# Kernel tuning notes

Measured on AMD Instinct MI355X. Metric: run time of the kernel, lower is better.

Reference implementation:

```python
import jax, jax.numpy as jnp
import numpy as np

K = 10                # knn neighbors
HEADS = 4             # attention heads
NAMES = ["self", "cross", "self", "cross", "self", "cross"]
SINKHORN_ITERS = 10


def _knn_graph_feature(x, k):
    # x: (b, c, n) -> (b, 2c, n, k), DGCNN-style graph feature
    xx = jnp.sum(x * x, axis=1)                              # (b, n)
    inner = jnp.einsum('bcn,bcm->bnm', x, x)
    dist = -xx[:, :, None] + 2.0 * inner - xx[:, None, :]    # negative squared L2
    idx = jax.lax.top_k(dist, k)[1]                          # (b, n, k)
    xt = jnp.transpose(x, (0, 2, 1))                         # (b, n, c)
    nbr = jax.vmap(lambda pts, id_: pts[id_])(xt, idx)       # (b, n, k, c)
    ctr = jnp.broadcast_to(xt[:, :, None, :], nbr.shape)
    feat = jnp.concatenate([nbr - ctr, ctr], axis=-1)        # (b, n, k, 2c)
    return jnp.transpose(feat, (0, 3, 1, 2))


def _encode(pts, w, b):
    # knn_feature: graph feature -> 1x1 conv2d -> mean over neighbors
    f = _knn_graph_feature(pts, K)                           # (b, 2c, n, k)
    y = jnp.einsum('oc,bcnk->bonk', w, f) + b[None, :, None, None]
    return y.mean(axis=-1)                                   # (b, d, n)


def _conv1(x, w, b):
    # 1x1 Conv1d
    return jnp.einsum('od,bdn->bon', w, x) + b[None, :, None]


def _bn(x, g, bt):
    # BatchNorm1d, training-mode batch statistics (biased var), eps=1e-5
    m = x.mean(axis=(0, 2), keepdims=True)
    v = ((x - m) ** 2).mean(axis=(0, 2), keepdims=True)
    return g[None, :, None] * (x - m) / jnp.sqrt(v + 1e-5) + bt[None, :, None]


def _mha(x, src, pw, pb, mw, mb):
    b, d, n = x.shape
    dim = d // HEADS
    q = _conv1(x, pw[0], pb[0]).reshape(b, dim, HEADS, -1)
    k = _conv1(src, pw[1], pb[1]).reshape(b, dim, HEADS, -1)
    v = _conv1(src, pw[2], pb[2]).reshape(b, dim, HEADS, -1)
    scores = jnp.einsum('bdhn,bdhm->bhnm', q, k) / (dim ** 0.5)
    prob = jax.nn.softmax(scores, axis=-1)
    out = jnp.einsum('bhnm,bdhm->bdhn', prob, v).reshape(b, d, -1)
    return _conv1(out, mw, mb)


def _prop(x, src, p):
    # AttentionalPropagation: MHA message + MLP([2d, 2d, d]) with BN+ReLU
    msg = _mha(x, src, p['pw'], p['pb'], p['mw'], p['mb'])
    y = jnp.concatenate([x, msg], axis=1)                    # (b, 2d, n)
    h = jax.nn.relu(_bn(_conv1(y, p['w1'], p['b1']), p['g'], p['bt']))
    return _conv1(h, p['w2'], p['b2'])


def _rodrigues(aa):
    # angle-axis (b,3) -> rotation matrices (b,3,3)
    theta = jnp.maximum(jnp.linalg.norm(aa, axis=-1, keepdims=True), 1e-8)
    r = aa / theta
    c = jnp.cos(theta)[..., None]
    s = jnp.sin(theta)[..., None]
    rx, ry, rz = r[..., 0], r[..., 1], r[..., 2]
    z = jnp.zeros_like(rx)
    Kmat = jnp.stack([jnp.stack([z, -rz, ry], -1),
                      jnp.stack([rz, z, -rx], -1),
                      jnp.stack([-ry, rx, z], -1)], -2)
    rrT = r[..., :, None] * r[..., None, :]
    I = jnp.eye(3, dtype=aa.dtype)
    return c * I + (1.0 - c) * rrT + s * Kmat


def reference(p2d, p3d, pose, enc2d_w, enc2d_b, enc3d_w, enc3d_b,
              proj_w, proj_b, merge_w, merge_b,
              mlp1_w, mlp1_b, bn_g, bn_b, mlp2_w, mlp2_b):
    # unit bearing vectors (assumption stated in weightedReprojectionErrorwithPose)
    f2 = p2d / jnp.linalg.norm(p2d, axis=-1, keepdims=True)
    desc0 = _encode(jnp.transpose(f2, (0, 2, 1)), enc2d_w, enc2d_b)   # (b, d, m)
    desc1 = _encode(jnp.transpose(p3d, (0, 2, 1)), enc3d_w, enc3d_b)  # (b, d, n)

    for i, name in enumerate(NAMES):
        p = dict(pw=proj_w[i], pb=proj_b[i], mw=merge_w[i], mb=merge_b[i],
                 w1=mlp1_w[i], b1=mlp1_b[i], g=bn_g[i], bt=bn_b[i],
                 w2=mlp2_w[i], b2=mlp2_b[i])
        s0, s1 = (desc1, desc0) if name == 'cross' else (desc0, desc1)
        d0 = desc0 + _prop(desc0, s0, p)
        d1 = desc1 + _prop(desc1, s1, p)
        desc0, desc1 = d0, d1

    # pairwiseL2Dist between descriptor sets
    f0 = jnp.transpose(desc0, (0, 2, 1))
    f1 = jnp.transpose(desc1, (0, 2, 1))
    n0 = jnp.sum(f0 * f0, -1)
    n1 = jnp.sum(f1 * f1, -1)
    dist2 = n0[:, :, None] + n1[:, None, :] - 2.0 * jnp.einsum('bmd,bnd->bmn', f0, f1)
    M = jnp.sqrt(jnp.clip(dist2, 1e-30, None))

    # log-space sinkhorn normalization -> joint weight matrix W
    log_alpha = -M
    for _ in range(SINKHORN_ITERS):
        log_alpha = log_alpha - jax.nn.logsumexp(log_alpha, axis=2, keepdims=True)
        log_alpha = log_alpha - jax.nn.logsumexp(log_alpha, axis=1, keepdims=True)
    W = jnp.exp(log_alpha)

    # weighted angular reprojection error at given pose (angle-axis + t)
    R = _rodrigues(pose[:, :3])
    t = pose[:, 3:]
    p3dt = jnp.einsum('bij,bnj->bni', R, p3d) + t[:, None, :]
    p3dt = p3dt / jnp.linalg.norm(p3dt, axis=-1, keepdims=True)
    err = jnp.einsum('bmn,bmn->b', W, 1.0 - jnp.einsum('bmd,bnd->bmn', f2, p3dt))
    return err


def setup_inputs() -> dict:
    key = jax.random.key(0)
    ks = jax.random.split(key, 12)
    B, Mpts, Npts, D, L = 4, 1024, 1024, 128, 6
    f = lambda k_, shp: jax.random.normal(k_, shp, dtype=jnp.float32) * 0.05
    return {
        'p2d': jax.random.normal(ks[0], (B, Mpts, 3), jnp.float32),
        'p3d': jax.random.normal(ks[1], (B, Npts, 3), jnp.float32),
        'pose': jax.random.normal(ks[2], (B, 6), jnp.float32) * 0.2,
        'enc2d_w': f(ks[3], (D, 6)), 'enc2d_b': jnp.zeros((D,), jnp.float32),
        'enc3d_w': f(ks[4], (D, 6)), 'enc3d_b': jnp.zeros((D,), jnp.float32),
        'proj_w': f(ks[5], (L, 3, D, D)), 'proj_b': jnp.zeros((L, 3, D), jnp.float32),
        'merge_w': f(ks[6], (L, D, D)), 'merge_b': jnp.zeros((L, D), jnp.float32),
        'mlp1_w': f(ks[7], (L, 2 * D, 2 * D)), 'mlp1_b': jnp.zeros((L, 2 * D), jnp.float32),
        'bn_g': jnp.ones((L, 2 * D), jnp.float32), 'bn_b': jnp.zeros((L, 2 * D), jnp.float32),
        'mlp2_w': f(ks[8], (L, D, 2 * D)), 'mlp2_b': jnp.zeros((L, D), jnp.float32),
    }
```

## Files before the change

kernel.cpp:

```cpp
#include <hip/hip_runtime.h>
#include <hip/hip_bf16.h>

constexpr int B   = 4;
constexpr int N   = 1024;
constexpr int D   = 128;
constexpr int KNN = 10;
constexpr int NH  = 4;

typedef _Float16 half2v __attribute__((ext_vector_type(2)));
typedef _Float16 f16x4  __attribute__((ext_vector_type(4)));
typedef _Float16 f16x8  __attribute__((ext_vector_type(8)));
typedef float    f32x4  __attribute__((ext_vector_type(4)));

static __device__ __forceinline__ half2v pkrtz(float a, float b) {
  return __builtin_bit_cast(half2v, __builtin_amdgcn_cvt_pkrtz(a, b));
}
static __device__ __forceinline__ float h2f(half2v h) {
  return __builtin_bit_cast(float, h);
}

__global__ __launch_bounds__(256) void k_norm2d(const float* __restrict__ p2d,
                                                float* __restrict__ f2) {
  int i = blockIdx.x * 256 + threadIdx.x;
  const float* p = p2d + (size_t)i * 3;
  float x = p[0], y = p[1], z = p[2];
  float inr = 1.f / sqrtf(x * x + y * y + z * z);
  float* o = f2 + (size_t)i * 3;
  o[0] = x * inr; o[1] = y * inr; o[2] = z * inr;
}

__global__ __launch_bounds__(256) void k_encode(const float* __restrict__ pts,
                                                const float* __restrict__ w,
                                                const float* __restrict__ bias,
                                                float* __restrict__ desc) {
  __shared__ float Px[N], Py[N], Pz[N], Xx[N];
  const int t = threadIdx.x;
  const int l = t & 63, wv = t >> 6;
  const int n = blockIdx.x * 4 + wv;
  const int b = blockIdx.y;
  const float* pb = pts + (size_t)b * N * 3;
  for (int i = t; i < N; i += 256) {
    float x = pb[i * 3 + 0], y = pb[i * 3 + 1], z = pb[i * 3 + 2];
    Px[i] = x; Py[i] = y; Pz[i] = z;
    Xx[i] = x * x + y * y + z * z;
  }
  __syncthreads();
  const float cx = Px[n], cy = Py[n], cz = Pz[n], cxx = Xx[n];
  float dist[16];
#pragma unroll
  for (int i = 0; i < 16; ++i) {
    int j = i * 64 + l;
    float ip = cx * Px[j] + cy * Py[j] + cz * Pz[j];
    dist[i] = 2.f * ip - cxx - Xx[j];
  }
  float sx = 0.f, sy = 0.f, sz = 0.f;
#pragma unroll
  for (int kk = 0; kk < KNN; ++kk) {
    float bv = dist[0]; int bi = l;
#pragma unroll
    for (int i = 1; i < 16; ++i) {
      if (dist[i] > bv) { bv = dist[i]; bi = i * 64 + l; }
    }
#pragma unroll
    for (int sft = 1; sft < 64; sft <<= 1) {
      float v2 = __shfl_xor(bv, sft, 64);
      int   i2 = __shfl_xor(bi, sft, 64);
      if (v2 > bv || (v2 == bv && i2 < bi)) { bv = v2; bi = i2; }
    }
    sx += Px[bi]; sy += Py[bi]; sz += Pz[bi];
    if ((bi & 63) == l) {
      int io = bi >> 6;
#pragma unroll
      for (int i = 0; i < 16; ++i)
        if (i == io) dist[i] = -3.0e38f;
    }
  }
  const float invk = 1.f / KNN;
  float feat[6];
  feat[0] = sx * invk - cx; feat[1] = sy * invk - cy; feat[2] = sz * invk - cz;
  feat[3] = cx; feat[4] = cy; feat[5] = cz;
#pragma unroll
  for (int rep = 0; rep < 2; ++rep) {
    int c = rep * 64 + l;
    const float* wr = w + c * 6;
    float a = bias[c];
#pragma unroll
    for (int j = 0; j < 6; ++j) a += wr[j] * feat[j];
    desc[((size_t)b * D + c) * N + n] = a;
  }
}

__global__ __launch_bounds__(256) void k_gemm(
    const float* __restrict__ pA0, const float* __restrict__ pA1,
    const float* __restrict__ pB0, const float* __restrict__ pB1,
    const float* __restrict__ w, const float* __restrict__ bias,
    const float* __restrict__ res, float* __restrict__ out,
    const float* __restrict__ stat, const float* __restrict__ g,
    const float* __restrict__ bt,
    int Cin, int catOff, size_t a_bstr, size_t b_bstr,
    int segCout, size_t segStride, int qkvMode) {
  __shared__ _Float16 As[64][48];
  __shared__ half2v   Bs[16][132];
  __shared__ float Ac[256], Bc[256];
  const int tid = threadIdx.x;
  const int wv  = tid >> 6;
  const int l   = tid & 63;
  const int wo  = wv >> 1;
  const int wn  = wv & 1;
  const int lr  = l & 15;
  const int lg  = l >> 4;
  const int o0 = blockIdx.y * 64;
  const int zb = blockIdx.x;
  const int z  = zb >> 3;
  const int n0 = (zb & 7) * 128;
  const int s = z >> 2, b = z & 3;
  const int seg = o0 / segCout;
  const int oo  = o0 % segCout;

  const float* XA = (s ? pA1 : pA0) + (size_t)b * a_bstr;
  const float* XB = pB0 ? ((s ? pB1 : pB0) + (size_t)b * b_bstr) : nullptr;
  const bool segB = qkvMode && (seg > 0);

  if (stat) {
    const float* st = stat + (size_t)s * 256 * 2;
    float A = st[tid * 2 + 1] * g[tid];
    Ac[tid] = A;
    Bc[tid] = fmaf(-st[tid * 2 + 0], A, bt[tid]);
  }

  f32x4 acc[2][4];
#pragma unroll
  for (int i = 0; i < 2; ++i)
#pragma unroll
    for (int j = 0; j < 4; ++j) acc[i][j] = (f32x4){0.f, 0.f, 0.f, 0.f};

  for (int kb = 0; kb < Cin; kb += 32) {
    __syncthreads();
#pragma unroll
    for (int j = 0; j < 2; ++j) {
      int idx = j * 256 + tid;
      int o = idx >> 3, c4 = (idx & 7) * 4;
      float4 wvv = *(const float4*)&w[(size_t)(o0 + o) * Cin + kb + c4];
      *(half2v*)&As[o][c4]     = pkrtz(wvv.x, wvv.y);
      *(half2v*)&As[o][c4 + 2] = pkrtz(wvv.z, wvv.w);
    }
#pragma unroll
    for (int j = 0; j < 2; ++j) {
      int idx = j * 256 + tid;
      int rp = idx >> 5, c4 = (idx & 31) * 4;
      int c0 = kb + 2 * rp, c1 = c0 + 1;
      const float* s0; int cc0 = c0;
      const float* s1; int cc1 = c1;
      if (qkvMode) {
        s0 = segB ? XB : XA; s1 = s0;
      } else {
        if (c0 >= catOff) { s0 = XB; cc0 = c0 - catOff; } else s0 = XA;
        if (c1 >= catOff) { s1 = XB; cc1 = c1 - catOff; } else s1 = XA;
      }
      float4 v0 = *(const float4*)&s0[(size_t)cc0 * N + n0 + c4];
      float4 v1 = *(const float4*)&s1[(size_t)cc1 * N + n0 + c4];
      if (stat) {
        float A0 = Ac[c0], B0 = Bc[c0], A1 = Ac[c1], B1 = Bc[c1];
        v0.x = fmaxf(fmaf(v0.x, A0, B0), 0.f);
        v0.y = fmaxf(fmaf(v0.y, A0, B0), 0.f);
        v0.z = fmaxf(fmaf(v0.z, A0, B0), 0.f);
        v0.w = fmaxf(fmaf(v0.w, A0, B0), 0.f);
        v1.x = fmaxf(fmaf(v1.x, A1, B1), 0.f);
        v1.y = fmaxf(fmaf(v1.y, A1, B1), 0.f);
        v1.z = fmaxf(fmaf(v1.z, A1, B1), 0.f);
        v1.w = fmaxf(fmaf(v1.w, A1, B1), 0.f);
      }
      float4 packed;
      packed.x = h2f(pkrtz(v0.x, v1.x));
      packed.y = h2f(pkrtz(v0.y, v1.y));
      packed.z = h2f(pkrtz(v0.z, v1.z));
      packed.w = h2f(pkrtz(v0.w, v1.w));
      *(float4*)&Bs[rp][c4] = packed;
    }
    __syncthreads();
    f16x8 afr0 = *(const f16x8*)&As[wo * 32 + lr][lg * 8];
    f16x8 afr1 = *(const f16x8*)&As[wo * 32 + 16 + lr][lg * 8];
#pragma unroll
    for (int tj = 0; tj < 4; ++tj) {
      int nn = wn * 64 + tj * 16 + lr;
      float4 btmp;
      btmp.x = *(const float*)&Bs[lg * 4 + 0][nn];
      btmp.y = *(const float*)&Bs[lg * 4 + 1][nn];
      btmp.z = *(const float*)&Bs[lg * 4 + 2][nn];
      btmp.w = *(const float*)&Bs[lg * 4 + 3][nn];
      f16x8 bfr = __builtin_bit_cast(f16x8, btmp);
      acc[0][tj] = __builtin_amdgcn_mfma_f32_16x16x32_f16(afr0, bfr, acc[0][tj], 0, 0, 0);
      acc[1][tj] = __builtin_amdgcn_mfma_f32_16x16x32_f16(afr1, bfr, acc[1][tj], 0, 0, 0);
    }
  }
#pragma unroll
  for (int ti = 0; ti < 2; ++ti) {
#pragma unroll
    for (int tj = 0; tj < 4; ++tj) {
      int nn = n0 + wn * 64 + tj * 16 + lr;
#pragma unroll
      for (int r = 0; r < 4; ++r) {
        int lrow = wo * 32 + ti * 16 + lg * 4 + r;
        size_t ob = (size_t)seg * segStride +
                    ((size_t)z * segCout + oo + lrow) * N + nn;
        float v = acc[ti][tj][r] + bias[o0 + lrow];
        if (res) v += res[ob];
        out[ob] = v;
      }
    }
  }
}

__global__ __launch_bounds__(512) void k_attn(const float* __restrict__ Q,
                                              const float* __restrict__ Kt,
                                              const float* __restrict__ Vt,
                                              float* __restrict__ O) {
  __shared__ _Float16 Klds[128][40];
  __shared__ _Float16 Vlds[32][136];
  const int t  = threadIdx.x;
  const int l  = t & 63, w = t >> 6;
  const int lr = l & 15, lg = l >> 4;
  const int q0 = blockIdx.x * 128 + w * 16;
  const int h  = blockIdx.y;
  const int z  = blockIdx.z;
  const size_t base = (size_t)z * (size_t)(D * N);
  const float* Kg = Kt + base + (size_t)h * N;
  const float* Vg = Vt + base + (size_t)h * N;
  const float scale = 0.17677669529663687f;

  f16x8 qfrag;
  {
    float qv[8];
#pragma unroll
    for (int j = 0; j < 8; ++j)
      qv[j] = Q[base + (size_t)((lg * 8 + j) * 4 + h) * N + q0 + lr] * scale;
    float4 qp;
    qp.x = h2f(pkrtz(qv[0], qv[1]));
    qp.y = h2f(pkrtz(qv[2], qv[3]));
    qp.z = h2f(pkrtz(qv[4], qv[5]));
    qp.w = h2f(pkrtz(qv[6], qv[7]));
    qfrag = __builtin_bit_cast(f16x8, qp);
  }

  f32x4 oacc0 = (f32x4){0.f, 0.f, 0.f, 0.f};
  f32x4 oacc1 = (f32x4){0.f, 0.f, 0.f, 0.f};
  float m = -1e30f, lsum = 0.f;

  for (int c = 0; c < 8; ++c) {
    const int k0 = c * 128;
    __syncthreads();
    {
      int kk = t & 127, d0 = (t >> 7) * 8;
      float kv[8];
#pragma unroll
      for (int j = 0; j < 8; ++j)
        kv[j] = Kg[(size_t)((d0 + j) * 4) * N + k0 + kk];
      float4 pk;
      pk.x = h2f(pkrtz(kv[0], kv[1]));
      pk.y = h2f(pkrtz(kv[2], kv[3]));
      pk.z = h2f(pkrtz(kv[4], kv[5]));
      pk.w = h2f(pkrtz(kv[6], kv[7]));
      *(float4*)&Klds[kk][d0] = pk;
      int dv = t & 31, ko = (t >> 5) * 8;
      const float* vp = Vg + (size_t)(dv * 4) * N + k0 + ko;
      float4 v0 = *(const float4*)vp;
      float4 v1 = *(const float4*)(vp + 4);
      float4 pv;
      pv.x = h2f(pkrtz(v0.x, v0.y)); pv.y = h2f(pkrtz(v0.z, v0.w));
      pv.z = h2f(pkrtz(v1.x, v1.y)); pv.w = h2f(pkrtz(v1.z, v1.w));
      *(float4*)&Vlds[dv][ko] = pv;
    }
    __syncthreads();
#pragma unroll
    for (int kt = 0; kt < 8; ++kt) {
      f16x8 kfrag = *(const f16x8*)&Klds[kt * 16 + lr][lg * 8];
      f32x4 s = __builtin_amdgcn_mfma_f32_16x16x32_f16(
          kfrag, qfrag, (f32x4){0.f, 0.f, 0.f, 0.f}, 0, 0, 0);
      float tmax = fmaxf(fmaxf(s[0], s[1]), fmaxf(s[2], s[3]));
      tmax = fmaxf(tmax, __shfl_xor(tmax, 16, 64));
      tmax = fmaxf(tmax, __shfl_xor(tmax, 32, 64));
      float nm = fmaxf(m, tmax);
      float corr = __expf(m - nm);
      m = nm;
      lsum *= corr;
#pragma unroll
      for (int r = 0; r < 4; ++r) { oacc0[r] *= corr; oacc1[r] *= corr; }
      float p0 = __expf(s[0] - m), p1 = __expf(s[1] - m);
      float p2 = __expf(s[2] - m), p3 = __expf(s[3] - m);
      float ts = p0 + p1 + p2 + p3;
      ts += __shfl_xor(ts, 16, 64);
      ts += __shfl_xor(ts, 32, 64);
      lsum += ts;
      float2 ptmp;
      ptmp.x = h2f(pkrtz(p0, p1));
      ptmp.y = h2f(pkrtz(p2, p3));
      f16x4 pfrag = __builtin_bit_cast(f16x4, ptmp);
      float2 vt0 = *(const float2*)&Vlds[lr][kt * 16 + lg * 4];
      float2 vt1 = *(const float2*)&Vlds[16 + lr][kt * 16 + lg * 4];
      f16x4 vf0 = __builtin_bit_cast(f16x4, vt0);
      f16x4 vf1 = __builtin_bit_cast(f16x4, vt1);
      oacc0 = __builtin_amdgcn_mfma_f32_16x16x16f16(vf0, pfrag, oacc0, 0, 0, 0);
      oacc1 = __builtin_amdgcn_mfma_f32_16x16x16f16(vf1, pfrag, oacc1, 0, 0, 0);
    }
  }
  float invL = 1.f / lsum;
#pragma unroll
  for (int r = 0; r < 4; ++r) {
    int d0 = lg * 4 + r;
    O[base + (size_t)(d0 * 4 + h) * N + q0 + lr] = oacc0[r] * invL;
    int d1 = 16 + lg * 4 + r;
    O[base + (size_t)(d1 * 4 + h) * N + q0 + lr] = oacc1[r] * invL;
  }
}

__global__ __launch_bounds__(256) void k_bnstat(const float* __restrict__ h,
                                                float* __restrict__ stat) {
  int c = blockIdx.x, s = blockIdx.y, t = threadIdx.x;
  __shared__ float red[256], red2[256];
  const float* base = h + ((size_t)s * B * 256 + c) * N;
  float sum = 0, sq = 0;
  for (int b = 0; b < B; ++b)
    for (int i = t; i < N; i += 256) {
      float v = base[(size_t)b * 256 * N + i];
      sum += v; sq = fmaf(v, v, sq);
    }
  red[t] = sum; red2[t] = sq; __syncthreads();
  for (int sft = 128; sft > 0; sft >>= 1) {
    if (t < sft) { red[t] += red[t + sft]; red2[t] += red2[t + sft]; }
    __syncthreads();
  }
  if (t == 0) {
    float mean = red[0] / (float)(B * N);
    float var = fmaxf(red2[0] / (float)(B * N) - mean * mean, 0.f);
    stat[(s * 256 + c) * 2 + 0] = mean;
    stat[(s * 256 + c) * 2 + 1] = 1.f / sqrtf(var + 1e-5f);
  }
}

__global__ __launch_bounds__(256) void k_dist(const float* __restrict__ d0,
                                              const float* __restrict__ d1,
                                              float* __restrict__ la) {
  __shared__ float xm[8][128];
  __shared__ float n0s[8];
  int m0 = blockIdx.x * 8, b = blockIdx.y, t = threadIdx.x;
  const float* p0 = d0 + (size_t)b * D * N;
  const float* p1 = d1 + (size_t)b * D * N;
  for (int i = t; i < 8 * 128; i += 256) {
    int mm = i >> 7, d = i & 127;
    xm[mm][d] = p0[(size_t)d * N + m0 + mm];
  }
  __syncthreads();
  if (t < 8) {
    float s = 0;
    for (int d = 0; d < 128; ++d) s += xm[t][d] * xm[t][d];
    n0s[t] = s;
  }
  __syncthreads();
  float dot[8][4] = {{0}};
  float n1[4] = {0, 0, 0, 0};
  for (int d = 0; d < 128; ++d) {
    float v[4];
#pragma unroll
    for (int u = 0; u < 4; ++u) {
      v[u] = p1[(size_t)d * N + t + u * 256];
      n1[u] = fmaf(v[u], v[u], n1[u]);
    }
#pragma unroll
    for (int mm = 0; mm < 8; ++mm) {
      float x = xm[mm][d];
#pragma unroll
      for (int u = 0; u < 4; ++u) dot[mm][u] = fmaf(x, v[u], dot[mm][u]);
    }
  }
  for (int mm = 0; mm < 8; ++mm) {
    float* row = la + ((size_t)b * N + m0 + mm) * N;
#pragma unroll
    for (int u = 0; u < 4; ++u) {
      float dist2 = fmaxf(n0s[mm] + n1[u] - 2.f * dot[mm][u], 1e-30f);
      row[t + u * 256] = -sqrtf(dist2);
    }
  }
}

__global__ __launch_bounds__(256) void k_row_r(const float* __restrict__ l0,
                                               const float* __restrict__ cvec,
                                               float* __restrict__ r,
                                               int useC) {
  __shared__ float red[256];
  int t = threadIdx.x;
  int bm = blockIdx.x;
  int b = bm >> 10;
  const float* row = l0 + (size_t)bm * N;
  float v0 = row[t], v1 = row[t + 256], v2 = row[t + 512], v3 = row[t + 768];
  if (useC) {
    const float* cl = cvec + (size_t)b * N;
    v0 -= cl[t]; v1 -= cl[t + 256]; v2 -= cl[t + 512]; v3 -= cl[t + 768];
  }
  float mx = fmaxf(fmaxf(v0, v1), fmaxf(v2, v3));
  red[t] = mx; __syncthreads();
  for (int s = 128; s > 0; s >>= 1) {
    if (t < s) red[t] = fmaxf(red[t], red[t + s]);
    __syncthreads();
  }
  mx = red[0]; __syncthreads();
  float se = __expf(v0 - mx) + __expf(v1 - mx) + __expf(v2 - mx) + __expf(v3 - mx);
  red[t] = se; __syncthreads();
  for (int s = 128; s > 0; s >>= 1) {
    if (t < s) red[t] += red[t + s];
    __syncthreads();
  }
  if (t == 0) r[bm] = mx + __logf(red[0]);
}

__global__ __launch_bounds__(256) void k_col_part(const float* __restrict__ l0,
                                                  const float* __restrict__ r,
                                                  float* __restrict__ pmax,
                                                  float* __restrict__ psum) {
  int t = threadIdx.x;
  int n = blockIdx.x * 256 + t;
  int p = blockIdx.y, b = blockIdx.z;
  const float* base = l0 + ((size_t)b * N + p * 32) * N + n;
  const float* rr = r + (size_t)b * N + p * 32;
  float mx = -1e30f, s = 0;
  for (int m = 0; m < 32; ++m) {
    float v = base[(size_t)m * N] - rr[m];
    if (v > mx) { s = s * __expf(mx - v) + 1.f; mx = v; }
    else s += __expf(v - mx);
  }
  pmax[((size_t)b * 32 + p) * N + n] = mx;
  psum[((size_t)b * 32 + p) * N + n] = s;
}

__global__ __launch_bounds__(256) void k_col_fin(const float* __restrict__ pmax,
                                                 const float* __restrict__ psum,
                                                 float* __restrict__ cvec) {
  int i = blockIdx.x * 256 + threadIdx.x;
  int b = i / N, n = i % N;
  float mx = -1e30f;
#pragma unroll
  for (int p = 0; p < 32; ++p) mx = fmaxf(mx, pmax[((size_t)b * 32 + p) * N + n]);
  float s = 0;
#pragma unroll
  for (int p = 0; p < 32; ++p)
    s += psum[((size_t)b * 32 + p) * N + n] * __expf(pmax[((size_t)b * 32 + p) * N + n] - mx);
  cvec[i] = mx + __logf(s);
}

__global__ __launch_bounds__(256) void k_rod(const float* __restrict__ pose,
                                             const float* __restrict__ p3d,
                                             float* __restrict__ p3dt) {
  int b = blockIdx.y;
  int n = blockIdx.x * 256 + threadIdx.x;
  const float* aa = pose + b * 6;
  float ax = aa[0], ay = aa[1], az = aa[2];
  float th = fmaxf(sqrtf(ax * ax + ay * ay + az * az), 1e-8f);
  float rx = ax / th, ry = ay / th, rz = az / th;
  float c = cosf(th), s = sinf(th), oc = 1.f - c;
  float R00 = c + oc * rx * rx,      R01 = oc * rx * ry - s * rz, R02 = oc * rx * rz + s * ry;
  float R10 = oc * ry * rx + s * rz, R11 = c + oc * ry * ry,      R12 = oc * ry * rz - s * rx;
  float R20 = oc * rz * rx - s * ry, R21 = oc * rz * ry + s * rx, R22 = c + oc * rz * rz;
  const float* p = p3d + ((size_t)b * N + n) * 3;
  float x = p[0], y = p[1], z = p[2];
  float X = R00 * x + R01 * y + R02 * z + aa[3];
  float Y = R10 * x + R11 * y + R12 * z + aa[4];
  float Z = R20 * x + R21 * y + R22 * z + aa[5];
  float inr = 1.f / sqrtf(X * X + Y * Y + Z * Z);
  float* o = p3dt + ((size_t)b * N + n) * 3;
  o[0] = X * inr; o[1] = Y * inr; o[2] = Z * inr;
}

__global__ __launch_bounds__(256) void k_err(const float* __restrict__ l0,
                                             const float* __restrict__ r,
                                             const float* __restrict__ cvec,
                                             const float* __restrict__ f2,
                                             const float* __restrict__ p3dt,
                                             float* __restrict__ rowsum) {
  __shared__ float red[256];
  int m = blockIdx.x, b = blockIdx.y, t = threadIdx.x;
  const float* row = l0 + ((size_t)b * N + m) * N;
  const float* cl = cvec + (size_t)b * N;
  const float rm = r[(size_t)b * N + m];
  const float* f = f2 + ((size_t)b * N + m) * 3;
  float fx = f[0], fy = f[1], fz = f[2];
  float s = 0;
  for (int n = t; n < N; n += 256) {
    const float* pp = p3dt + ((size_t)b * N + n) * 3;
    float dot = fx * pp[0] + fy * pp[1] + fz * pp[2];
    s += __expf(row[n] - rm - cl[n]) * (1.f - dot);
  }
  red[t] = s; __syncthreads();
  for (int sft = 128; sft > 0; sft >>= 1) {
    if (t < sft) red[t] += red[t + sft];
    __syncthreads();
  }
  if (t == 0) rowsum[(size_t)b * N + m] = red[0];
}

__global__ __launch_bounds__(256) void k_err_fin(const float* __restrict__ rowsum,
                                                 float* __restrict__ out) {
  __shared__ float red[256];
  int b = blockIdx.x, t = threadIdx.x;
  float s = 0;
  for (int i = t; i < N; i += 256) s += rowsum[(size_t)b * N + i];
  red[t] = s; __syncthreads();
  for (int sft = 128; sft > 0; sft >>= 1) {
    if (t < sft) red[t] += red[t + sft];
    __syncthreads();
  }
  if (t == 0) out[b] = red[0];
}

extern "C" void kernel_launch(void* const* d_in, const int* in_sizes, int n_in,
                              void* d_out, int out_size, void* d_ws, size_t ws_size,
                              hipStream_t stream) {
  const float* p2d     = (const float*)d_in[0];
  const float* p3d     = (const float*)d_in[1];
  const float* pose    = (const float*)d_in[2];
  const float* enc2d_w = (const float*)d_in[3];
  const float* enc2d_b = (const float*)d_in[4];
  const float* enc3d_w = (const float*)d_in[5];
  const float* enc3d_b = (const float*)d_in[6];
  const float* proj_w  = (const float*)d_in[7];
  const float* proj_b  = (const float*)d_in[8];
  const float* merge_w = (const float*)d_in[9];
  const float* merge_b = (const float*)d_in[10];
  const float* mlp1_w  = (const float*)d_in[11];
  const float* mlp1_b  = (const float*)d_in[12];
  const float* bn_g    = (const float*)d_in[13];
  const float* bn_b    = (const float*)d_in[14];
  const float* mlp2_w  = (const float*)d_in[15];
  const float* mlp2_b  = (const float*)d_in[16];

  float* W = (float*)d_ws;
  size_t off = 0;
  auto alloc = [&](size_t nelem) { float* p = W + off; off += nelem; return p; };
  const size_t SET = (size_t)B * D * N;
  float* f2    = alloc((size_t)B * N * 3);
  float* p3dt  = alloc((size_t)B * N * 3);
  float* descA = alloc(2 * SET);
  float* descB = alloc(2 * SET);
  float* qkv   = alloc(3 * 2 * SET);
  float* attnb = alloc(2 * SET);
  float* msgb  = alloc(2 * SET);
  float* hb    = alloc((size_t)2 * B * 256 * N);
  float* stat  = alloc(2 * 256 * 2);
  float* la    = alloc((size_t)B * N * N);
  float* pmax  = alloc((size_t)B * 32 * N);
  float* psum  = alloc((size_t)B * 32 * N);
  float* cvec  = alloc((size_t)B * N);
  float* rvec  = alloc((size_t)B * N);
  float* rowsum= alloc((size_t)B * N);
  (void)ws_size; (void)in_sizes; (void)n_in; (void)out_size;

  float* Qb = qkv;
  float* Kb = qkv + 2 * SET;
  float* Vb = qkv + 4 * SET;
  const size_t DS = (size_t)D * N;

  k_norm2d<<<(B * N) / 256, 256, 0, stream>>>(p2d, f2);
  k_encode<<<dim3(N / 4, B), 256, 0, stream>>>(f2, enc2d_w, enc2d_b, descA);
  k_encode<<<dim3(N / 4, B), 256, 0, stream>>>(p3d, enc3d_w, enc3d_b, descA + SET);

  float* dc = descA;
  float* dn = descB;
  for (int i = 0; i < 6; ++i) {
    int cross = (i & 1);
    const float* pw = proj_w + (size_t)i * 3 * D * D;
    const float* pb = proj_b + (size_t)i * 3 * D;
    float* d0 = dc;
    float* d1 = dc + SET;
    const float* sA = cross ? d1 : d0;
    const float* sB = cross ? d0 : d1;

    k_gemm<<<dim3(64, 6), 256, 0, stream>>>(
        d0, d1, sA, sB, pw, pb, nullptr, qkv, nullptr, nullptr, nullptr,
        D, D, DS, DS, D, 2 * SET, 1);
    k_attn<<<dim3(N / 128, NH, 2 * B), 512, 0, stream>>>(Qb, Kb, Vb, attnb);
    k_gemm<<<dim3(64, 2), 256, 0, stream>>>(
        attnb, attnb + SET, nullptr, nullptr, merge_w + (size_t)i * D * D,
        merge_b + (size_t)i * D, nullptr, msgb, nullptr, nullptr, nullptr,
        D, D, DS, DS, D, 0, 0);
    k_gemm<<<dim3(64, 4), 256, 0, stream>>>(
        dc, dc + SET, msgb, msgb + SET, mlp1_w + (size_t)i * 256 * 256,
        mlp1_b + (size_t)i * 256, nullptr, hb, nullptr, nullptr, nullptr,
        256, 128, DS, DS, 256, 0, 0);
    k_bnstat<<<dim3(256, 2), 256, 0, stream>>>(hb, stat);
    k_gemm<<<dim3(64, 2), 256, 0, stream>>>(
        hb, hb + (size_t)B * 256 * N, nullptr, nullptr,
        mlp2_w + (size_t)i * D * 256, mlp2_b + (size_t)i * D, dc, dn,
        stat, bn_g + (size_t)i * 256, bn_b + (size_t)i * 256,
        256, 256, (size_t)256 * N, 0, D, 0, 0);
    float* tmp = dc; dc = dn; dn = tmp;
  }

  k_dist<<<dim3(N / 8, B), 256, 0, stream>>>(dc, dc + SET, la);
  for (int it = 0; it < 10; ++it) {
    k_row_r<<<B * N, 256, 0, stream>>>(la, cvec, rvec, it > 0 ? 1 : 0);
    k_col_part<<<dim3(N / 256, 32, B), 256, 0, stream>>>(la, rvec, pmax, psum);
    k_col_fin<<<(B * N) / 256, 256, 0, stream>>>(pmax, psum, cvec);
  }
  k_rod<<<dim3(N / 256, B), 256, 0, stream>>>(pose, p3d, p3dt);
  k_err<<<dim3(N, B), 256, 0, stream>>>(la, rvec, cvec, f2, p3dt, rowsum);
  k_err_fin<<<B, 256, 0, stream>>>(rowsum, (float*)d_out);
}
```

Baseline: 874.7 us.

## Fuse Sinkhorn row logsumexp and column partial reduction into one tiled kernel

Replaces the separate row-normalizer kernel and column-partial kernel with a single kernel. Each block handles a 16-row tile, computes the row logsumexp with an online max/sum and wave shuffles, then reuses the same tile (likely still in cache) to produce column partials. This halves the number of launches per iteration and the number of reads of the cost matrix. In exchange, the column finish step now reduces over 64 partials instead of 32, and only 256 blocks are launched per iteration.

```diff
diff --git a/kernel.cpp b/kernel.cpp
--- a/kernel.cpp
+++ b/kernel.cpp
@@ -382,53 +382,69 @@
   }
 }
 
-__global__ __launch_bounds__(256) void k_row_r(const float* __restrict__ l0,
-                                               const float* __restrict__ cvec,
-                                               float* __restrict__ r,
-                                               int useC) {
-  __shared__ float red[256];
-  int t = threadIdx.x;
-  int bm = blockIdx.x;
-  int b = bm >> 10;
-  const float* row = l0 + (size_t)bm * N;
-  float v0 = row[t], v1 = row[t + 256], v2 = row[t + 512], v3 = row[t + 768];
-  if (useC) {
-    const float* cl = cvec + (size_t)b * N;
-    v0 -= cl[t]; v1 -= cl[t + 256]; v2 -= cl[t + 512]; v3 -= cl[t + 768];
-  }
-  float mx = fmaxf(fmaxf(v0, v1), fmaxf(v2, v3));
-  red[t] = mx; __syncthreads();
-  for (int s = 128; s > 0; s >>= 1) {
-    if (t < s) red[t] = fmaxf(red[t], red[t + s]);
-    __syncthreads();
-  }
-  mx = red[0]; __syncthreads();
-  float se = __expf(v0 - mx) + __expf(v1 - mx) + __expf(v2 - mx) + __expf(v3 - mx);
-  red[t] = se; __syncthreads();
-  for (int s = 128; s > 0; s >>= 1) {
-    if (t < s) red[t] += red[t + s];
-    __syncthreads();
-  }
-  if (t == 0) r[bm] = mx + __logf(red[0]);
-}
-
-__global__ __launch_bounds__(256) void k_col_part(const float* __restrict__ l0,
-                                                  const float* __restrict__ r,
-                                                  float* __restrict__ pmax,
-                                                  float* __restrict__ psum) {
-  int t = threadIdx.x;
-  int n = blockIdx.x * 256 + t;
-  int p = blockIdx.y, b = blockIdx.z;
-  const float* base = l0 + ((size_t)b * N + p * 32) * N + n;
-  const float* rr = r + (size_t)b * N + p * 32;
-  float mx = -1e30f, s = 0;
-  for (int m = 0; m < 32; ++m) {
-    float v = base[(size_t)m * N] - rr[m];
-    if (v > mx) { s = s * __expf(mx - v) + 1.f; mx = v; }
-    else s += __expf(v - mx);
-  }
-  pmax[((size_t)b * 32 + p) * N + n] = mx;
-  psum[((size_t)b * 32 + p) * N + n] = s;
+__global__ __launch_bounds__(256) void k_sink(const float* __restrict__ l0,
+                                              const float* __restrict__ cvec,
+                                              float* __restrict__ rvec,
+                                              float* __restrict__ pmax,
+                                              float* __restrict__ psum,
+                                              int useC) {
+  __shared__ float rsh[16];
+  const int t = threadIdx.x;
+  const int row = t >> 4, ln = t & 15;
+  const int p = blockIdx.x, b = blockIdx.y;
+  const int m0 = p * 16;
+  const float* tile = l0 + ((size_t)b * N + m0) * N;
+  const float* cl = cvec + (size_t)b * N;
+
+  float mx = -1e30f, s = 0.f;
+  const float* rp = tile + (size_t)row * N;
+#pragma unroll 4
+  for (int i = 0; i < 16; ++i) {
+    int n4 = (ln + i * 16) * 4;
+    float4 v = *(const float4*)&rp[n4];
+    if (useC) {
+      const float4 c4 = *(const float4*)&cl[n4];
+      v.x -= c4.x; v.y -= c4.y; v.z -= c4.z; v.w -= c4.w;
+    }
+    float tm = fmaxf(fmaxf(v.x, v.y), fmaxf(v.z, v.w));
+    if (tm > mx) { s *= __expf(mx - tm); mx = tm; }
+    s += __expf(v.x - mx) + __expf(v.y - mx) + __expf(v.z - mx) + __expf(v.w - mx);
+  }
+#pragma unroll
+  for (int sft = 1; sft < 16; sft <<= 1) {
+    float m2 = __shfl_xor(mx, sft, 64);
+    float s2 = __shfl_xor(s, sft, 64);
+    float nm = fmaxf(mx, m2);
+    s = s * __expf(mx - nm) + s2 * __expf(m2 - nm);
+    mx = nm;
+  }
+  float r = mx + __logf(s);
+  if (ln == 0) {
+    rsh[row] = r;
+    rvec[(size_t)b * N + m0 + row] = r;
+  }
+  __syncthreads();
+  float rloc[16];
+#pragma unroll
+  for (int m = 0; m < 16; ++m) rloc[m] = rsh[m];
+  const int n4 = t * 4;
+  float cmx[4] = {-1e30f, -1e30f, -1e30f, -1e30f};
+  float cs[4]  = {0.f, 0.f, 0.f, 0.f};
+#pragma unroll 4
+  for (int m = 0; m < 16; ++m) {
+    float4 v = *(const float4*)&tile[(size_t)m * N + n4];
+    float vv[4] = {v.x - rloc[m], v.y - rloc[m], v.z - rloc[m], v.w - rloc[m]};
+#pragma unroll
+    for (int u = 0; u < 4; ++u) {
+      if (vv[u] > cmx[u]) { cs[u] = cs[u] * __expf(cmx[u] - vv[u]) + 1.f; cmx[u] = vv[u]; }
+      else cs[u] += __expf(vv[u] - cmx[u]);
+    }
+  }
+  float4 om, os;
+  om.x = cmx[0]; om.y = cmx[1]; om.z = cmx[2]; om.w = cmx[3];
+  os.x = cs[0];  os.y = cs[1];  os.z = cs[2];  os.w = cs[3];
+  *(float4*)&pmax[((size_t)b * 64 + p) * N + n4] = om;
+  *(float4*)&psum[((size_t)b * 64 + p) * N + n4] = os;
 }
 
 __global__ __launch_bounds__(256) void k_col_fin(const float* __restrict__ pmax,
@@ -437,12 +453,12 @@
   int i = blockIdx.x * 256 + threadIdx.x;
   int b = i / N, n = i % N;
   float mx = -1e30f;
-#pragma unroll
-  for (int p = 0; p < 32; ++p) mx = fmaxf(mx, pmax[((size_t)b * 32 + p) * N + n]);
+#pragma unroll 8
+  for (int p = 0; p < 64; ++p) mx = fmaxf(mx, pmax[((size_t)b * 64 + p) * N + n]);
   float s = 0;
-#pragma unroll
-  for (int p = 0; p < 32; ++p)
-    s += psum[((size_t)b * 32 + p) * N + n] * __expf(pmax[((size_t)b * 32 + p) * N + n] - mx);
+#pragma unroll 8
+  for (int p = 0; p < 64; ++p)
+    s += psum[((size_t)b * 64 + p) * N + n] * __expf(pmax[((size_t)b * 64 + p) * N + n] - mx);
   cvec[i] = mx + __logf(s);
 }
 
@@ -545,8 +561,8 @@
   float* hb    = alloc((size_t)2 * B * 256 * N);
   float* stat  = alloc(2 * 256 * 2);
   float* la    = alloc((size_t)B * N * N);
-  float* pmax  = alloc((size_t)B * 32 * N);
-  float* psum  = alloc((size_t)B * 32 * N);
+  float* pmax  = alloc((size_t)B * 64 * N);
+  float* psum  = alloc((size_t)B * 64 * N);
   float* cvec  = alloc((size_t)B * N);
   float* rvec  = alloc((size_t)B * N);
   float* rowsum= alloc((size_t)B * N);
@@ -595,8 +611,8 @@
 
   k_dist<<<dim3(N / 8, B), 256, 0, stream>>>(dc, dc + SET, la);
   for (int it = 0; it < 10; ++it) {
-    k_row_r<<<B * N, 256, 0, stream>>>(la, cvec, rvec, it > 0 ? 1 : 0);
-    k_col_part<<<dim3(N / 256, 32, B), 256, 0, stream>>>(la, rvec, pmax, psum);
+    k_sink<<<dim3(64, B), 256, 0, stream>>>(la, cvec, rvec, pmax, psum,
+                                            it > 0 ? 1 : 0);
     k_col_fin<<<(B * N) / 256, 256, 0, stream>>>(pmax, psum, cvec);
   }
   k_rod<<<dim3(N / 256, B), 256, 0, stream>>>(pose, p3d, p3dt);
```

New measurement: 967.7 us. 1.11x slower.

## Fold merge projection into first MLP layer weights to remove a GEMM

Applied to the files above, without the earlier changes.

Precomputes, once per call, a combined weight matrix by multiplying the message half of mlp1 by the merge conv weight and folding the merge bias into the mlp1 bias. The MLP first-layer GEMM then reads the attention output directly, which removes the merge GEMM launch and the msgb round trip through memory in each of the six layers. It adds a small fold kernel per call and slightly changes floating-point rounding order.

```diff
diff --git a/kernel.cpp b/kernel.cpp
--- a/kernel.cpp
+++ b/kernel.cpp
@@ -27,6 +27,34 @@
   float inr = 1.f / sqrtf(x * x + y * y + z * z);
   float* o = f2 + (size_t)i * 3;
   o[0] = x * inr; o[1] = y * inr; o[2] = z * inr;
+}
+
+__global__ __launch_bounds__(128) void k_fold(const float* __restrict__ mlp1_w,
+                                              const float* __restrict__ mlp1_b,
+                                              const float* __restrict__ merge_w,
+                                              const float* __restrict__ merge_b,
+                                              float* __restrict__ wcomb,
+                                              float* __restrict__ bcomb) {
+  __shared__ float red[128];
+  const int o = blockIdx.x;
+  const int i = blockIdx.y;
+  const int c = threadIdx.x;
+  const float* W1 = mlp1_w + (size_t)i * 256 * 256 + (size_t)o * 256;
+  const float* Wm = merge_w + (size_t)i * 128 * 128;
+  float* out = wcomb + (size_t)i * 256 * 256 + (size_t)o * 256;
+  out[c] = W1[c];
+  float acc = 0.f;
+#pragma unroll 8
+  for (int k = 0; k < 128; ++k)
+    acc = fmaf(W1[128 + k], Wm[(size_t)k * 128 + c], acc);
+  out[128 + c] = acc;
+  red[c] = W1[128 + c] * merge_b[i * 128 + c];
+  __syncthreads();
+  for (int s = 64; s > 0; s >>= 1) {
+    if (c < s) red[c] += red[c + s];
+    __syncthreads();
+  }
+  if (c == 0) bcomb[i * 256 + o] = mlp1_b[i * 256 + o] + red[0];
 }
 
 __global__ __launch_bounds__(256) void k_encode(const float* __restrict__ pts,
@@ -541,7 +569,6 @@
   float* descB = alloc(2 * SET);
   float* qkv   = alloc(3 * 2 * SET);
   float* attnb = alloc(2 * SET);
-  float* msgb  = alloc(2 * SET);
   float* hb    = alloc((size_t)2 * B * 256 * N);
   float* stat  = alloc(2 * 256 * 2);
   float* la    = alloc((size_t)B * N * N);
@@ -550,12 +577,17 @@
   float* cvec  = alloc((size_t)B * N);
   float* rvec  = alloc((size_t)B * N);
   float* rowsum= alloc((size_t)B * N);
+  float* wcomb = alloc((size_t)6 * 256 * 256);
+  float* bcomb = alloc((size_t)6 * 256);
   (void)ws_size; (void)in_sizes; (void)n_in; (void)out_size;
 
   float* Qb = qkv;
   float* Kb = qkv + 2 * SET;
   float* Vb = qkv + 4 * SET;
   const size_t DS = (size_t)D * N;
+
+  k_fold<<<dim3(256, 6), 128, 0, stream>>>(mlp1_w, mlp1_b, merge_w, merge_b,
+                                           wcomb, bcomb);
 
   k_norm2d<<<(B * N) / 256, 256, 0, stream>>>(p2d, f2);
   k_encode<<<dim3(N / 4, B), 256, 0, stream>>>(f2, enc2d_w, enc2d_b, descA);
@@ -576,13 +608,9 @@
         d0, d1, sA, sB, pw, pb, nullptr, qkv, nullptr, nullptr, nullptr,
         D, D, DS, DS, D, 2 * SET, 1);
     k_attn<<<dim3(N / 128, NH, 2 * B), 512, 0, stream>>>(Qb, Kb, Vb, attnb);
-    k_gemm<<<dim3(64, 2), 256, 0, stream>>>(
-        attnb, attnb + SET, nullptr, nullptr, merge_w + (size_t)i * D * D,
-        merge_b + (size_t)i * D, nullptr, msgb, nullptr, nullptr, nullptr,
-        D, D, DS, DS, D, 0, 0);
     k_gemm<<<dim3(64, 4), 256, 0, stream>>>(
-        dc, dc + SET, msgb, msgb + SET, mlp1_w + (size_t)i * 256 * 256,
-        mlp1_b + (size_t)i * 256, nullptr, hb, nullptr, nullptr, nullptr,
+        dc, dc + SET, attnb, attnb + SET, wcomb + (size_t)i * 256 * 256,
+        bcomb + (size_t)i * 256, nullptr, hb, nullptr, nullptr, nullptr,
         256, 128, DS, DS, 256, 0, 0);
     k_bnstat<<<dim3(256, 2), 256, 0, stream>>>(hb, stat);
     k_gemm<<<dim3(64, 2), 256, 0, stream>>>(
```

Measured after the change: 826.4 us, median of 2. -5.5%, faster.
